# Kernel tuning notes

Measured on AMD Instinct MI355X. Metric: run time of the kernel, lower is better.

## Reference

```python
import jax, jax.numpy as jnp
import numpy as np

B, D, G, F, A = 262144, 128, 8, 80, 18  # batch, obs dim, n_games, n_features, max_actions


def setup_inputs() -> dict:
    key = jax.random.key(0)
    ks = jax.random.split(key, 10)
    s1 = 1.0 / np.sqrt(D)
    s2 = 1.0 / np.sqrt(F)
    state = jax.random.normal(ks[0], (B, D), dtype=jnp.float32)
    idx = jnp.sort(jax.random.randint(ks[1], (B,), 0, G, dtype=jnp.int32))
    W1 = jax.random.normal(ks[2], (G, F, D), dtype=jnp.float32) * s1
    b1 = jax.random.normal(ks[3], (G, F), dtype=jnp.float32) * s1
    W2 = jax.random.normal(ks[4], (F, F), dtype=jnp.float32) * s2
    b2 = jax.random.normal(ks[5], (F,), dtype=jnp.float32) * s2
    W3 = jax.random.normal(ks[6], (F, F), dtype=jnp.float32) * s2
    b3 = jax.random.normal(ks[7], (F,), dtype=jnp.float32) * s2
    W4 = jax.random.normal(ks[8], (G, A, F), dtype=jnp.float32) * s2
    b4 = jax.random.normal(ks[9], (G, A), dtype=jnp.float32) * s2
    return {"state": state, "idx": idx, "W1": W1, "b1": b1, "W2": W2, "b2": b2,
            "W3": W3, "b3": b3, "W4": W4, "b4": b4}


def reference(state, idx, W1, b1, W2, b2, W3, b3, W4, b4):
    state = state.astype(jnp.float32)
    n_games = W1.shape[0]
    # Routed first layer: each sample goes through its game's Linear(D->F).
    # Loop is over the small fixed set of games; batch dim stays vectorized.
    h1 = jnp.zeros((state.shape[0], W1.shape[1]), dtype=state.dtype)
    for g in range(n_games):
        hg = state @ W1[g].T + b1[g]  # [B, F]
        h1 = h1 + jnp.where((idx == g)[:, None], hg, jnp.zeros((), state.dtype))
    h1 = jax.nn.relu(h1)
    # Shared MLP (features == 'relu')
    h = jax.nn.relu(h1 @ W2.T + b2)
    h = jax.nn.relu(h @ W3.T + b3)
    # All per-game heads, stacked: q[b, g, a]
    q = jnp.einsum('bf,gaf->bga', h, W4) + b4  # [B, G, A]
    # Gather the head matching each sample's game (action=None branch)
    q_idx = jnp.take_along_axis(q, idx[:, None, None].astype(jnp.int32), axis=1)  # [B,1,A]
    return jnp.squeeze(q_idx, axis=1)  # [B, A]
```

## Files before the change

kernel.cpp:

```cpp
#include <hip/hip_runtime.h>


#define B_TOT   262144
#define DDIM    128
#define NGAMES  8
#define FDIM    80
#define ADIM    18
#define MT      64
#define SD      136
#define SH      104
#define KP      96

#define W1O     0
#define W2O     81920
#define W3O     89600
#define W4O     97280
#define WTOT    121856

typedef __attribute__((ext_vector_type(8))) short short8;
typedef __attribute__((ext_vector_type(4))) short short4v;
typedef __attribute__((ext_vector_type(4))) float floatx4;

static __device__ __forceinline__ unsigned short f2bf(float f) {
  union { float f; unsigned u; } v; v.f = f;
  unsigned r = v.u + 0x7fffu + ((v.u >> 16) & 1u);
  return (unsigned short)(r >> 16);
}

__global__ void convert_weights(const float* __restrict__ W1, const float* __restrict__ W2,
                                const float* __restrict__ W3, const float* __restrict__ W4,
                                unsigned short* __restrict__ ws) {
  int t = blockIdx.x * 256 + threadIdx.x;
  if (t < W2O) {
    ws[t] = f2bf(W1[t]);
  } else if (t < W3O) {
    int i = t - W2O, n = i / KP, k = i - n * KP;
    ws[t] = (k < FDIM) ? f2bf(W2[n * FDIM + k]) : (unsigned short)0;
  } else if (t < W4O) {
    int i = t - W3O, n = i / KP, k = i - n * KP;
    ws[t] = (k < FDIM) ? f2bf(W3[n * FDIM + k]) : (unsigned short)0;
  } else if (t < WTOT) {
    int i = t - W4O, g = i / (32 * KP), r = i - g * (32 * KP);
    int n = r / KP, k = r - n * KP;
    ws[t] = (n < ADIM && k < FDIM) ? f2bf(W4[(g * ADIM + n) * FDIM + k]) : (unsigned short)0;
  }
}

static __device__ __forceinline__ void mlp_layer(
    const unsigned short* sIn, unsigned short* sOut,
    const unsigned short* __restrict__ Wbf, const float* __restrict__ bias,
    int rowbase, int l16, int quad)
{
  floatx4 acc[5];
#pragma unroll
  for (int ct = 0; ct < 5; ++ct) acc[ct] = (floatx4){0.f, 0.f, 0.f, 0.f};
#pragma unroll
  for (int ks = 0; ks < 3; ++ks) {
    int k0 = ks * 32 + quad * 8;
    short8 a = *(const short8*)(sIn + (rowbase + l16) * SH + k0);
    short8 bf[5];
#pragma unroll
    for (int ct = 0; ct < 5; ++ct)
      bf[ct] = *(const short8*)(Wbf + (ct * 16 + l16) * KP + k0);
#pragma unroll
    for (int ct = 0; ct < 5; ++ct)
      acc[ct] = __builtin_amdgcn_mfma_f32_16x16x32_bf16(a, bf[ct], acc[ct], 0, 0, 0);
  }
#pragma unroll
  for (int ct = 0; ct < 5; ++ct) {
    int col = ct * 16 + l16;
    float bv = bias[col];
#pragma unroll
    for (int r = 0; r < 4; ++r) {
      int row = rowbase + quad * 4 + r;
      float v = fmaxf(acc[ct][r] + bv, 0.f);
      sOut[row * SH + col] = f2bf(v);
    }
  }
}

__global__ __launch_bounds__(256, 5) void gym_fused(
    const float* __restrict__ state, const int* __restrict__ idx,
    const unsigned short* __restrict__ wbf,
    const float* __restrict__ b1, const float* __restrict__ b2,
    const float* __restrict__ b3, const float* __restrict__ b4,
    float* __restrict__ out)
{
  __shared__ __align__(16) unsigned short s_state[MT * SD];
  __shared__ __align__(16) unsigned short s_bufA[MT * SH];
  __shared__ int s_idx[MT];

  const int tid  = threadIdx.x;
  const int lane = tid & 63;
  const int wv   = tid >> 6;
  const int l16  = lane & 15;
  const int quad = lane >> 4;
  const int rowbase = wv * 16;
  const size_t blk_row0 = (size_t)blockIdx.x * MT;
  const short8 zero8 = {0, 0, 0, 0, 0, 0, 0, 0};

  {
    const float* gsrc = state + blk_row0 * DDIM;
#pragma unroll
    for (int i = 0; i < 8; ++i) {
      int c = i * 256 + tid;
      int r = c >> 5, cc = c & 31;
      floatx4 v = *(const floatx4*)(gsrc + c * 4);
      short4v s;
      s[0] = (short)f2bf(v[0]); s[1] = (short)f2bf(v[1]);
      s[2] = (short)f2bf(v[2]); s[3] = (short)f2bf(v[3]);
      *(short4v*)(s_state + r * SD + cc * 4) = s;
    }
  }
  if (tid < MT) s_idx[tid] = idx[blk_row0 + tid];
  if (tid < 128) {
    int r = tid >> 1, cc = tid & 1;
    *(short8*)(s_bufA + r * SH + 80 + cc * 8) = zero8;
  }
  __syncthreads();

  const int g_lo = s_idx[0];
  const int g_hi = s_idx[MT - 1];

  for (int g = g_lo; g <= g_hi; ++g) {
    floatx4 acc[5];
#pragma unroll
    for (int ct = 0; ct < 5; ++ct) acc[ct] = (floatx4){0.f, 0.f, 0.f, 0.f};
    const unsigned short* w1g = wbf + W1O + g * (FDIM * DDIM);
#pragma unroll
    for (int ks = 0; ks < 4; ++ks) {
      int k0 = ks * 32 + quad * 8;
      short8 a = *(const short8*)(s_state + (rowbase + l16) * SD + k0);
      short8 bf[5];
#pragma unroll
      for (int ct = 0; ct < 5; ++ct)
        bf[ct] = *(const short8*)(w1g + (ct * 16 + l16) * DDIM + k0);
#pragma unroll
      for (int ct = 0; ct < 5; ++ct)
        acc[ct] = __builtin_amdgcn_mfma_f32_16x16x32_bf16(a, bf[ct], acc[ct], 0, 0, 0);
    }
#pragma unroll
    for (int ct = 0; ct < 5; ++ct) {
      int col = ct * 16 + l16;
      float bv = b1[g * FDIM + col];
#pragma unroll
      for (int r = 0; r < 4; ++r) {
        int row = rowbase + quad * 4 + r;
        if (s_idx[row] == g) {
          float v = fmaxf(acc[ct][r] + bv, 0.f);
          s_bufA[row * SH + col] = f2bf(v);
        }
      }
    }
  }
  __syncthreads();

  unsigned short* s_h2 = s_state;
  if (lane < 32) {
    int r = rowbase + (lane >> 1), cc = lane & 1;
    *(short8*)(s_h2 + r * SH + 80 + cc * 8) = zero8;
  }

  mlp_layer(s_bufA, s_h2,  wbf + W2O, b2, rowbase, l16, quad);
  mlp_layer(s_h2,  s_bufA, wbf + W3O, b3, rowbase, l16, quad);

  for (int g = g_lo; g <= g_hi; ++g) {
    floatx4 acc[2];
#pragma unroll
    for (int ct = 0; ct < 2; ++ct) acc[ct] = (floatx4){0.f, 0.f, 0.f, 0.f};
    const unsigned short* w4g = wbf + W4O + g * (32 * KP);
#pragma unroll
    for (int ks = 0; ks < 3; ++ks) {
      int k0 = ks * 32 + quad * 8;
      short8 a = *(const short8*)(s_bufA + (rowbase + l16) * SH + k0);
      short8 bf[2];
#pragma unroll
      for (int ct = 0; ct < 2; ++ct)
        bf[ct] = *(const short8*)(w4g + (ct * 16 + l16) * KP + k0);
#pragma unroll
      for (int ct = 0; ct < 2; ++ct)
        acc[ct] = __builtin_amdgcn_mfma_f32_16x16x32_bf16(a, bf[ct], acc[ct], 0, 0, 0);
    }
#pragma unroll
    for (int ct = 0; ct < 2; ++ct) {
      int col = ct * 16 + l16;
      if (col < ADIM) {
        float bv = b4[g * ADIM + col];
#pragma unroll
        for (int r = 0; r < 4; ++r) {
          int row = rowbase + quad * 4 + r;
          if (s_idx[row] == g)
            out[(blk_row0 + row) * ADIM + col] = acc[ct][r] + bv;
        }
      }
    }
  }
}

extern "C" void kernel_launch(void* const* d_in, const int* in_sizes, int n_in,
                              void* d_out, int out_size, void* d_ws, size_t ws_size,
                              hipStream_t stream) {
  const float* state = (const float*)d_in[0];
  const int*   idx   = (const int*)d_in[1];
  const float* W1    = (const float*)d_in[2];
  const float* b1    = (const float*)d_in[3];
  const float* W2    = (const float*)d_in[4];
  const float* b2    = (const float*)d_in[5];
  const float* W3    = (const float*)d_in[6];
  const float* b3    = (const float*)d_in[7];
  const float* W4    = (const float*)d_in[8];
  const float* b4    = (const float*)d_in[9];
  float*       out   = (float*)d_out;
  unsigned short* wbf = (unsigned short*)d_ws;

  convert_weights<<<(WTOT + 255) / 256, 256, 0, stream>>>(W1, W2, W3, W4, wbf);
  gym_fused<<<B_TOT / MT, 256, 0, stream>>>(state, idx, wbf, b1, b2, b3, b4, out);
}
```

Measured before the change: 266.2 us.

## Load state fragments directly to registers and make each wave independent

The block-wide shared-memory staging of state is replaced by per-lane global loads that convert straight into MFMA A fragments held in registers. Each wave now owns a private 16-row shared buffer, and the MLP layers run in place, so all __syncthreads disappear. Routing indices are read per lane from global memory, and the game range is computed per wave rather than per block. LDS use drops a lot, which allows higher occupancy, but the state loads become strided 32-byte chunks per lane instead of fully coalesced rows. The in-place layers read their whole input into registers before writing, and within a wave this ordering relies on lockstep execution.

```diff
diff --git a/kernel.cpp b/kernel.cpp
--- a/kernel.cpp
+++ b/kernel.cpp
@@ -6,8 +6,8 @@
 #define NGAMES  8
 #define FDIM    80
 #define ADIM    18
+#define ROWS_W  16
 #define MT      64
-#define SD      136
 #define SH      104
 #define KP      96
 
@@ -18,7 +18,6 @@
 #define WTOT    121856
 
 typedef __attribute__((ext_vector_type(8))) short short8;
-typedef __attribute__((ext_vector_type(4))) short short4v;
 typedef __attribute__((ext_vector_type(4))) float floatx4;
 
 static __device__ __forceinline__ unsigned short f2bf(float f) {
@@ -46,25 +45,39 @@
   }
 }
 
-static __device__ __forceinline__ void mlp_layer(
-    const unsigned short* sIn, unsigned short* sOut,
-    const unsigned short* __restrict__ Wbf, const float* __restrict__ bias,
-    int rowbase, int l16, int quad)
+static __device__ __forceinline__ short8 ld_frag8_f32(const float* p) {
+  floatx4 a = *(const floatx4*)p;
+  floatx4 b = *(const floatx4*)(p + 4);
+  short8 r;
+  r[0] = (short)f2bf(a[0]); r[1] = (short)f2bf(a[1]);
+  r[2] = (short)f2bf(a[2]); r[3] = (short)f2bf(a[3]);
+  r[4] = (short)f2bf(b[0]); r[5] = (short)f2bf(b[1]);
+  r[6] = (short)f2bf(b[2]); r[7] = (short)f2bf(b[3]);
+  return r;
+}
+
+static __device__ __forceinline__ void mlp_layer_inplace(
+    unsigned short* hbuf,
+    const unsigned short* __restrict__ Wbf,
+    const float* __restrict__ bias,
+    int l16, int quad)
 {
+  short8 a[3];
+#pragma unroll
+  for (int ks = 0; ks < 3; ++ks)
+    a[ks] = *(const short8*)(hbuf + l16 * SH + ks * 32 + quad * 8);
+
   floatx4 acc[5];
 #pragma unroll
   for (int ct = 0; ct < 5; ++ct) acc[ct] = (floatx4){0.f, 0.f, 0.f, 0.f};
 #pragma unroll
   for (int ks = 0; ks < 3; ++ks) {
     int k0 = ks * 32 + quad * 8;
-    short8 a = *(const short8*)(sIn + (rowbase + l16) * SH + k0);
-    short8 bf[5];
-#pragma unroll
-    for (int ct = 0; ct < 5; ++ct)
-      bf[ct] = *(const short8*)(Wbf + (ct * 16 + l16) * KP + k0);
-#pragma unroll
-    for (int ct = 0; ct < 5; ++ct)
-      acc[ct] = __builtin_amdgcn_mfma_f32_16x16x32_bf16(a, bf[ct], acc[ct], 0, 0, 0);
+#pragma unroll
+    for (int ct = 0; ct < 5; ++ct) {
+      short8 bf = *(const short8*)(Wbf + (ct * 16 + l16) * KP + k0);
+      acc[ct] = __builtin_amdgcn_mfma_f32_16x16x32_bf16(a[ks], bf, acc[ct], 0, 0, 0);
+    }
   }
 #pragma unroll
   for (int ct = 0; ct < 5; ++ct) {
@@ -72,9 +85,8 @@
     float bv = bias[col];
 #pragma unroll
     for (int r = 0; r < 4; ++r) {
-      int row = rowbase + quad * 4 + r;
-      float v = fmaxf(acc[ct][r] + bv, 0.f);
-      sOut[row * SH + col] = f2bf(v);
+      int row = quad * 4 + r;
+      hbuf[row * SH + col] = f2bf(fmaxf(acc[ct][r] + bv, 0.f));
     }
   }
 }
@@ -86,41 +98,35 @@
     const float* __restrict__ b3, const float* __restrict__ b4,
     float* __restrict__ out)
 {
-  __shared__ __align__(16) unsigned short s_state[MT * SD];
-  __shared__ __align__(16) unsigned short s_bufA[MT * SH];
-  __shared__ int s_idx[MT];
+  __shared__ __align__(16) unsigned short s_h[4][ROWS_W * SH];
 
   const int tid  = threadIdx.x;
   const int lane = tid & 63;
   const int wv   = tid >> 6;
   const int l16  = lane & 15;
   const int quad = lane >> 4;
-  const int rowbase = wv * 16;
-  const size_t blk_row0 = (size_t)blockIdx.x * MT;
+  unsigned short* hbuf = s_h[wv];
+  const size_t row0 = (size_t)blockIdx.x * MT + wv * ROWS_W;
   const short8 zero8 = {0, 0, 0, 0, 0, 0, 0, 0};
 
+  int idxr[4];
+#pragma unroll
+  for (int r = 0; r < 4; ++r) idxr[r] = idx[row0 + quad * 4 + r];
+  const int g_lo = idx[row0];
+  const int g_hi = idx[row0 + ROWS_W - 1];
+
+  if (lane < 32) {
+    int r = lane >> 1, cc = lane & 1;
+    *(short8*)(hbuf + r * SH + 80 + cc * 8) = zero8;
+  }
+
+  short8 afrag[4];
   {
-    const float* gsrc = state + blk_row0 * DDIM;
-#pragma unroll
-    for (int i = 0; i < 8; ++i) {
-      int c = i * 256 + tid;
-      int r = c >> 5, cc = c & 31;
-      floatx4 v = *(const floatx4*)(gsrc + c * 4);
-      short4v s;
-      s[0] = (short)f2bf(v[0]); s[1] = (short)f2bf(v[1]);
-      s[2] = (short)f2bf(v[2]); s[3] = (short)f2bf(v[3]);
-      *(short4v*)(s_state + r * SD + cc * 4) = s;
-    }
-  }
-  if (tid < MT) s_idx[tid] = idx[blk_row0 + tid];
-  if (tid < 128) {
-    int r = tid >> 1, cc = tid & 1;
-    *(short8*)(s_bufA + r * SH + 80 + cc * 8) = zero8;
-  }
-  __syncthreads();
-
-  const int g_lo = s_idx[0];
-  const int g_hi = s_idx[MT - 1];
+    const float* sp = state + (row0 + l16) * DDIM + quad * 8;
+#pragma unroll
+    for (int ks = 0; ks < 4; ++ks)
+      afrag[ks] = ld_frag8_f32(sp + ks * 32);
+  }
 
   for (int g = g_lo; g <= g_hi; ++g) {
     floatx4 acc[5];
@@ -130,14 +136,11 @@
 #pragma unroll
     for (int ks = 0; ks < 4; ++ks) {
       int k0 = ks * 32 + quad * 8;
-      short8 a = *(const short8*)(s_state + (rowbase + l16) * SD + k0);
-      short8 bf[5];
-#pragma unroll
-      for (int ct = 0; ct < 5; ++ct)
-        bf[ct] = *(const short8*)(w1g + (ct * 16 + l16) * DDIM + k0);
-#pragma unroll
-      for (int ct = 0; ct < 5; ++ct)
-        acc[ct] = __builtin_amdgcn_mfma_f32_16x16x32_bf16(a, bf[ct], acc[ct], 0, 0, 0);
+#pragma unroll
+      for (int ct = 0; ct < 5; ++ct) {
+        short8 bf = *(const short8*)(w1g + (ct * 16 + l16) * DDIM + k0);
+        acc[ct] = __builtin_amdgcn_mfma_f32_16x16x32_bf16(afrag[ks], bf, acc[ct], 0, 0, 0);
+      }
     }
 #pragma unroll
     for (int ct = 0; ct < 5; ++ct) {
@@ -145,24 +148,21 @@
       float bv = b1[g * FDIM + col];
 #pragma unroll
       for (int r = 0; r < 4; ++r) {
-        int row = rowbase + quad * 4 + r;
-        if (s_idx[row] == g) {
-          float v = fmaxf(acc[ct][r] + bv, 0.f);
-          s_bufA[row * SH + col] = f2bf(v);
+        if (idxr[r] == g) {
+          int row = quad * 4 + r;
+          hbuf[row * SH + col] = f2bf(fmaxf(acc[ct][r] + bv, 0.f));
         }
       }
     }
   }
-  __syncthreads();
-
-  unsigned short* s_h2 = s_state;
-  if (lane < 32) {
-    int r = rowbase + (lane >> 1), cc = lane & 1;
-    *(short8*)(s_h2 + r * SH + 80 + cc * 8) = zero8;
-  }
-
-  mlp_layer(s_bufA, s_h2,  wbf + W2O, b2, rowbase, l16, quad);
-  mlp_layer(s_h2,  s_bufA, wbf + W3O, b3, rowbase, l16, quad);
+
+  mlp_layer_inplace(hbuf, wbf + W2O, b2, l16, quad);
+  mlp_layer_inplace(hbuf, wbf + W3O, b3, l16, quad);
+
+  short8 a3[3];
+#pragma unroll
+  for (int ks = 0; ks < 3; ++ks)
+    a3[ks] = *(const short8*)(hbuf + l16 * SH + ks * 32 + quad * 8);
 
   for (int g = g_lo; g <= g_hi; ++g) {
     floatx4 acc[2];
@@ -172,14 +172,11 @@
 #pragma unroll
     for (int ks = 0; ks < 3; ++ks) {
       int k0 = ks * 32 + quad * 8;
-      short8 a = *(const short8*)(s_bufA + (rowbase + l16) * SH + k0);
-      short8 bf[2];
-#pragma unroll
-      for (int ct = 0; ct < 2; ++ct)
-        bf[ct] = *(const short8*)(w4g + (ct * 16 + l16) * KP + k0);
-#pragma unroll
-      for (int ct = 0; ct < 2; ++ct)
-        acc[ct] = __builtin_amdgcn_mfma_f32_16x16x32_bf16(a, bf[ct], acc[ct], 0, 0, 0);
+#pragma unroll
+      for (int ct = 0; ct < 2; ++ct) {
+        short8 bf = *(const short8*)(w4g + (ct * 16 + l16) * KP + k0);
+        acc[ct] = __builtin_amdgcn_mfma_f32_16x16x32_bf16(a3[ks], bf, acc[ct], 0, 0, 0);
+      }
     }
 #pragma unroll
     for (int ct = 0; ct < 2; ++ct) {
@@ -188,9 +185,8 @@
         float bv = b4[g * ADIM + col];
 #pragma unroll
         for (int r = 0; r < 4; ++r) {
-          int row = rowbase + quad * 4 + r;
-          if (s_idx[row] == g)
-            out[(blk_row0 + row) * ADIM + col] = acc[ct][r] + bv;
+          if (idxr[r] == g)
+            out[(row0 + quad * 4 + r) * ADIM + col] = acc[ct][r] + bv;
         }
       }
     }
```

Measured after the change: 275.0 us. 3.3% more time.
